# Optimization experiments

Measured on AMD Instinct MI355X. Metric: run time of the kernel, lower is better.

The kernel has to match this reference:

```python
import jax, jax.numpy as jnp
import numpy as np

N_NODES = 50000
N_EDGES = 800000
NODE_IN = 16
NODE_OUT = 3
H = 128
N_LAYERS = 3


def setup_inputs() -> dict:
    key = jax.random.key(0)
    ks = jax.random.split(key, 16)
    s = 0.05
    inp = {
        "x": jax.random.normal(ks[0], (N_NODES, NODE_IN), dtype=jnp.float32),
        "edge_index": jax.random.randint(ks[1], (2, N_EDGES), 0, N_NODES, dtype=jnp.int64),
        # encoder / decoder
        "enc_w": jax.random.normal(ks[2], (NODE_IN, H), dtype=jnp.float32) * s,
        "enc_b": jnp.zeros((H,), dtype=jnp.float32),
        "dec_w": jax.random.normal(ks[3], (H, NODE_OUT), dtype=jnp.float32) * s,
        "dec_b": jnp.zeros((NODE_OUT,), dtype=jnp.float32),
        # 3 processor layers, edge MLP: Linear(2H,H) -> ReLU -> Linear(H,H)
        "edge_w1": jax.random.normal(ks[4], (N_LAYERS, 2 * H, H), dtype=jnp.float32) * s,
        "edge_b1": jnp.zeros((N_LAYERS, H), dtype=jnp.float32),
        "edge_w2": jax.random.normal(ks[5], (N_LAYERS, H, H), dtype=jnp.float32) * s,
        "edge_b2": jnp.zeros((N_LAYERS, H), dtype=jnp.float32),
        # node MLP: Linear(2H,H) -> ReLU -> Linear(H,H)
        "node_w1": jax.random.normal(ks[6], (N_LAYERS, 2 * H, H), dtype=jnp.float32) * s,
        "node_b1": jnp.zeros((N_LAYERS, H), dtype=jnp.float32),
        "node_w2": jax.random.normal(ks[7], (N_LAYERS, H, H), dtype=jnp.float32) * s,
        "node_b2": jnp.zeros((N_LAYERS, H), dtype=jnp.float32),
    }
    return inp


def reference(x, edge_index, enc_w, enc_b, dec_w, dec_b,
              edge_w1, edge_b1, edge_w2, edge_b2,
              node_w1, node_b1, node_w2, node_b2):
    row = edge_index[0]  # source nodes
    col = edge_index[1]  # destination nodes
    h = x @ enc_w + enc_b  # [N, H]
    for l in range(N_LAYERS):
        # EdgeModel: cat(src, dest) -> MLP
        e_in = jnp.concatenate([h[row], h[col]], axis=1)  # [E, 2H]
        e = jnp.maximum(e_in @ edge_w1[l] + edge_b1[l], 0.0) @ edge_w2[l] + edge_b2[l]  # [E, H]
        # NodeModel: scatter_add messages by col, cat with x -> MLP
        agg = jax.ops.segment_sum(e, col, num_segments=h.shape[0])  # [N, H]
        n_in = jnp.concatenate([h, agg], axis=1)  # [N, 2H]
        h_upd = jnp.maximum(n_in @ node_w1[l] + node_b1[l], 0.0) @ node_w2[l] + node_b2[l]
        h = h + h_upd  # residual
    return h @ dec_w + dec_b  # [N, NODE_OUT]
```

## Files before the change

### kernel.cpp

```cpp
#include <hip/hip_runtime.h>
#include <hip/hip_bf16.h>
#include <stdint.h>

#define N_NODES 50000
#define N_EDGES 800000
#define HID 128
#define NODE_IN 16
#define NODE_OUT 3
#define NODE_TILES 782
#define SCAN_BLOCKS 196
#define EDGE_BLOCKS 3125
#define MFOLD_BLOCKS 192
#define DG 32
#define DBLOCKS 1563

typedef __attribute__((ext_vector_type(8))) short short8;
typedef __attribute__((ext_vector_type(4))) float f32x4;
typedef __attribute__((ext_vector_type(4))) unsigned int u32x4;

__device__ __forceinline__ unsigned short f2bf(float f) {
    union { float f; unsigned int u; } v; v.f = f;
    unsigned int u = v.u;
    u += 0x7fff + ((u >> 16) & 1);
    return (unsigned short)(u >> 16);
}
__device__ __forceinline__ float bf2f(unsigned short s) {
    union { unsigned int u; float f; } v; v.u = ((unsigned int)s) << 16;
    return v.f;
}
__device__ __forceinline__ float bfu_lo(unsigned int u) {
    union { unsigned int u; float f; } v; v.u = u << 16; return v.f;
}
__device__ __forceinline__ float bfu_hi(unsigned int u) {
    union { unsigned int u; float f; } v; v.u = u & 0xffff0000u; return v.f;
}
__device__ __forceinline__ unsigned int cvt_pk_bf16(float lo, float hi) {
    unsigned int r;
    asm("v_cvt_pk_bf16_f32 %0, %1, %2" : "=v"(r) : "v"(lo), "v"(hi));
    return r;
}

__global__ __launch_bounds__(256) void k1_hist_mfold(
    const int* __restrict__ colp, int* __restrict__ cnt, int* __restrict__ rank,
    const float* __restrict__ edge_w2, const float* __restrict__ node_w1,
    const float* __restrict__ edge_b2,
    float* __restrict__ Mtmp, float* __restrict__ Vtmp) {
    int b = blockIdx.x, t = threadIdx.x;
    if (b < EDGE_BLOCKS) {
        int e = b * 256 + t;
        rank[e] = atomicAdd(&cnt[colp[e]], 1);
    } else {
        int d = (b - EDGE_BLOCKS) * 256 + t;
        int L = d / 16384, rem = d & 16383;
        int k = rem >> 7, n = rem & 127;
        const float* w2  = edge_w2 + (size_t)L * 16384;
        const float* w1b = node_w1 + (size_t)L * 32768 + 16384;
        float acc = 0.f;
        #pragma unroll 4
        for (int j = 0; j < 128; j++) acc += w2[k * 128 + j] * w1b[j * 128 + n];
        Mtmp[d] = acc;
        if (k == 0) {
            const float* b2 = edge_b2 + (size_t)L * 128;
            float vv = 0.f;
            #pragma unroll 4
            for (int j = 0; j < 128; j++) vv += b2[j] * w1b[j * 128 + n];
            Vtmp[L * 128 + n] = vv;
        }
    }
}

__global__ __launch_bounds__(256) void k2a_scan1_swizzle(
    const int* __restrict__ cnt, int* __restrict__ ex, int* __restrict__ bsums,
    const float* __restrict__ edge_w1, const float* __restrict__ node_w1,
    const float* __restrict__ node_w2, const float* __restrict__ Mtmp,
    unsigned short* __restrict__ swz) {
    __shared__ int s[256];
    int b = blockIdx.x, t = threadIdx.x;
    if (b < SCAN_BLOCKS) {
        int i = b * 256 + t;
        int v = (i < N_NODES) ? cnt[i] : 0;
        s[t] = v;
        __syncthreads();
        for (int off = 1; off < 256; off <<= 1) {
            int u = (t >= off) ? s[t - off] : 0;
            __syncthreads();
            s[t] += u;
            __syncthreads();
        }
        if (i < N_NODES) ex[i] = s[t] - v;
        if (t == 255) bsums[b] = s[255];
    } else {
        for (int d = (b - SCAN_BLOCKS) * 256 + t; d < 3 * 98304;
             d += (gridDim.x - SCAN_BLOCKS) * 256) {
            int L = d / 98304;
            int rem = d - L * 98304;
            unsigned short* base = swz + L * 98304;
            if (rem < 32768) {
                const float* w1 = edge_w1 + (size_t)L * 32768;
                int j = rem & 7, ll = (rem >> 3) & 63, tt = rem >> 9;
                int nt = tt & 15, kt = tt >> 4;
                int k = kt * 32 + ((ll >> 4) << 3) + j;
                int cc = nt * 16 + (ll & 15);
                float v = (cc < 128) ? w1[k * 128 + cc] : w1[(128 + k) * 128 + (cc - 128)];
                base[rem] = f2bf(v);
            } else if (rem < 49152) {
            } else if (rem < 81920) {
                int d2 = rem - 49152;
                int j = d2 & 7, ll = (d2 >> 3) & 63, tt = d2 >> 9;
                int nt = tt & 7, kt = tt >> 3;
                int k = kt * 32 + ((ll >> 4) << 3) + j, n = (nt << 4) + (ll & 15);
                float v = (k < 128) ? node_w1[(size_t)L * 32768 + k * 128 + n]
                                    : Mtmp[(size_t)L * 16384 + (k - 128) * 128 + n];
                base[rem] = f2bf(v);
            } else {
                int d2 = rem - 81920;
                const float* src = node_w2 + (size_t)L * 16384;
                int j = d2 & 7, ll = (d2 >> 3) & 63, tt = d2 >> 9;
                int nt = tt & 7, kt = tt >> 3;
                int k = kt * 32 + ((ll >> 4) << 3) + j, n = (nt << 4) + (ll & 15);
                base[rem] = f2bf(src[k * 128 + n]);
            }
        }
    }
}

__global__ __launch_bounds__(256) void k3a_scatter(
    const int* __restrict__ rowp, const int* __restrict__ colp,
    const int* __restrict__ ex, const int* __restrict__ bsums,
    const int* __restrict__ rank, int* __restrict__ rsrt,
    int* __restrict__ ex2) {
    __shared__ int sc[256];
    __shared__ int ls[SCAN_BLOCKS];
    int t = threadIdx.x;
    int v = (t < SCAN_BLOCKS) ? bsums[t] : 0;
    sc[t] = v;
    __syncthreads();
    for (int off = 1; off < 256; off <<= 1) {
        int u = (t >= off) ? sc[t - off] : 0;
        __syncthreads();
        sc[t] += u;
        __syncthreads();
    }
    if (t < SCAN_BLOCKS) ls[t] = sc[t] - v;
    __syncthreads();

    int b = blockIdx.x;
    if (b < SCAN_BLOCKS) {
        int i = b * 256 + t;
        if (i < N_NODES) ex2[i] = ex[i] + ls[b];
    }

    int e = b * 256 + t;
    if (e >= N_EDGES) return;
    int c = colp[e];
    int pos = ex[c] + ls[c >> 8] + rank[e];
    rsrt[pos] = rowp[e];
}

__global__ __launch_bounds__(256, 4) void k3b_encoder_sd(
    const float* __restrict__ x, const float* __restrict__ enc_w, const float* __restrict__ enc_b,
    const unsigned short* __restrict__ w1c, const float* __restrict__ eb1,
    unsigned short* __restrict__ h,
    unsigned short* __restrict__ S, unsigned short* __restrict__ D)
{
    __shared__ float wts[NODE_IN * HID];
    __shared__ float bts[HID];
    __shared__ float xs[64][NODE_IN];
    __shared__ unsigned short hs[64][136];
    int t = threadIdx.x, wave = t >> 6, l = t & 63, q = l >> 4, l16 = l & 15;
    int n0 = blockIdx.x * 64;
    int nt0s = wave * 4;

    for (int i = t; i < NODE_IN * HID; i += 256) wts[i] = enc_w[i];
    if (t < HID) bts[t] = enc_b[t];
    for (int i = t; i < 64 * NODE_IN; i += 256) {
        int nl = i >> 4, ii = i & 15;
        int n = n0 + nl;
        xs[nl][ii] = (n < N_NODES) ? x[n * NODE_IN + ii] : 0.f;
    }
    short8 wr[4][4];
    #pragma unroll
    for (int kt = 0; kt < 4; kt++)
        #pragma unroll
        for (int i = 0; i < 4; i++)
            wr[kt][i] = *(const short8*)(w1c + ((kt * 16 + nt0s + i) * 64 + l) * 8);
    __syncthreads();

    for (int o = t; o < 64 * HID; o += 256) {
        int nl = o >> 7, cc = o & 127;
        float acc = bts[cc];
        #pragma unroll
        for (int i = 0; i < NODE_IN; i++) acc += xs[nl][i] * wts[i * HID + cc];
        unsigned short hb = f2bf(acc);
        hs[nl][cc] = hb;
        int n = n0 + nl;
        if (n < N_NODES) h[n * HID + cc] = hb;
    }
    __syncthreads();

    f32x4 acc[4][4];
    #pragma unroll
    for (int g = 0; g < 4; g++)
        #pragma unroll
        for (int i = 0; i < 4; i++) acc[g][i] = (f32x4){0.f, 0.f, 0.f, 0.f};
    #pragma unroll
    for (int kt = 0; kt < 4; kt++) {
        #pragma unroll
        for (int g = 0; g < 4; g++) {
            short8 a = *(const short8*)&hs[g * 16 + l16][kt * 32 + q * 8];
            #pragma unroll
            for (int i = 0; i < 4; i++)
                acc[g][i] = __builtin_amdgcn_mfma_f32_16x16x32_bf16(a, wr[kt][i], acc[g][i], 0, 0, 0);
        }
    }
    #pragma unroll
    for (int i = 0; i < 4; i++) {
        int cc = (nt0s + i) * 16 + l16;
        float badd = 0.f;
        if (cc >= 128) badd = eb1[cc - 128];
        #pragma unroll
        for (int g = 0; g < 4; g++)
            #pragma unroll
            for (int r = 0; r < 4; r++) {
                int n = n0 + g * 16 + q * 4 + r;
                if (n < N_NODES) {
                    unsigned short v = f2bf(acc[g][i][r] + badd);
                    if (cc < 128) S[n * HID + cc] = v;
                    else          D[n * HID + (cc - 128)] = v;
                }
            }
    }
}

__global__ __launch_bounds__(256, 8) void edge_kernel(
    const unsigned short* __restrict__ S, const unsigned short* __restrict__ D,
    const int* __restrict__ rsrt, const int* __restrict__ ex2,
    float* __restrict__ aggH)
{
    int t = threadIdx.x;
    int g16 = t >> 4, ch = t & 15;

    const int q = DBLOCKS / 8, r = DBLOCKS % 8;
    int xcd = blockIdx.x & 7, slot = blockIdx.x >> 3;
    int cntx = q + (xcd < r);
    if (slot >= cntx) return;
    int myb = xcd * q + (xcd < r ? xcd : r) + slot;

    int dbase = myb * DG + g16 * 2;

    #pragma unroll
    for (int di = 0; di < 2; di++) {
        int d = dbase + di;
        if (d >= N_NODES) break;
        int e0 = ex2[d];
        int e1 = (d + 1 < N_NODES) ? ex2[d + 1] : N_EDGES;

        short8 dv = *(const short8*)(D + (size_t)d * HID + ch * 8);
        float dr[8];
        #pragma unroll
        for (int p = 0; p < 4; p++) {
            unsigned int ud = ((const unsigned int*)&dv)[p];
            dr[2 * p]     = bfu_lo(ud);
            dr[2 * p + 1] = bfu_hi(ud);
        }

        float a[8];
        #pragma unroll
        for (int j = 0; j < 8; j++) a[j] = 0.f;

        int e = e0;
        short8 sv_n = (short8){0,0,0,0,0,0,0,0};
        if (e < e1) {
            int rn = rsrt[e];
            sv_n = *(const short8*)(S + (size_t)rn * HID + ch * 8);
        }
        while (e < e1) {
            short8 sv = sv_n;
            int en = e + 1;
            if (en < e1) {
                int rn = rsrt[en];
                sv_n = *(const short8*)(S + (size_t)rn * HID + ch * 8);
            }
            #pragma unroll
            for (int p = 0; p < 4; p++) {
                unsigned int us = ((const unsigned int*)&sv)[p];
                float v0 = bfu_lo(us) + dr[2 * p];
                float v1 = bfu_hi(us) + dr[2 * p + 1];
                v0 = v0 > 0.f ? v0 : 0.f;
                v1 = v1 > 0.f ? v1 : 0.f;
                a[2 * p]     += v0;
                a[2 * p + 1] += v1;
            }
            e = en;
        }

        f32x4* dst = (f32x4*)(aggH + (size_t)d * HID + ch * 8);
        dst[0] = (f32x4){a[0], a[1], a[2], a[3]};
        dst[1] = (f32x4){a[4], a[5], a[6], a[7]};
    }
}

template<int LAST>
__global__ __launch_bounds__(256, 4) void node_kernel(
    unsigned short* __restrict__ h, float* __restrict__ aggH, const int* __restrict__ cnt,
    const unsigned short* __restrict__ w1m_s, const float* __restrict__ b1,
    const float* __restrict__ vfold,
    const unsigned short* __restrict__ w2s, const float* __restrict__ b2,
    const unsigned short* __restrict__ w1c_next, const float* __restrict__ eb1n,
    unsigned short* __restrict__ S, unsigned short* __restrict__ D,
    const float* __restrict__ dec_w, const float* __restrict__ dec_b, float* __restrict__ out)
{
    __shared__ unsigned short in_h[64][136];
    __shared__ unsigned short in_a[64][136];
    __shared__ int cnt_s[64];
    __shared__ float dw[HID * NODE_OUT];
    __shared__ float db[NODE_OUT];
    int t = threadIdx.x, wave = t >> 6, l = t & 63, q = l >> 4, l16 = l & 15;
    int nt0 = wave * 2, nt0s = wave * 4;
    int n0 = blockIdx.x * 64;

    if (LAST) {
        for (int i = t; i < HID * NODE_OUT; i += 256) dw[i] = dec_w[i];
        if (t < NODE_OUT) db[t] = dec_b[t];
    }

    #pragma unroll
    for (int it = 0; it < 8; it++) {
        int g = it * 256 + t;
        int nl = g >> 5, sub = g & 31, half = sub >> 4, li = sub & 15;
        int n = n0 + nl;
        short8 v = (short8){0, 0, 0, 0, 0, 0, 0, 0};
        if (n < N_NODES) {
            if (half == 0) {
                v = *(const short8*)(h + n * HID + li * 8);
            } else {
                const float* ap = aggH + n * HID + li * 8;
                f32x4 a0 = *(const f32x4*)ap, a1 = *(const f32x4*)(ap + 4);
                unsigned int* vp = (unsigned int*)&v;
                vp[0] = cvt_pk_bf16(a0[0], a0[1]);
                vp[1] = cvt_pk_bf16(a0[2], a0[3]);
                vp[2] = cvt_pk_bf16(a1[0], a1[1]);
                vp[3] = cvt_pk_bf16(a1[2], a1[3]);
            }
        }
        if (half == 0) *(short8*)&in_h[nl][li * 8] = v;
        else           *(short8*)&in_a[nl][li * 8] = v;
    }
    if (t < 64) cnt_s[t] = (n0 + t < N_NODES) ? cnt[n0 + t] : 0;
    __syncthreads();

    float b1r0 = b1[nt0 * 16 + l16], b1r1 = b1[(nt0 + 1) * 16 + l16];
    float vr0 = vfold[nt0 * 16 + l16], vr1 = vfold[(nt0 + 1) * 16 + l16];
    float b2r0 = b2[nt0 * 16 + l16], b2r1 = b2[(nt0 + 1) * 16 + l16];

    f32x4 acc[4][2];
    #pragma unroll
    for (int g = 0; g < 4; g++)
        #pragma unroll
        for (int j = 0; j < 2; j++) acc[g][j] = (f32x4){0.f, 0.f, 0.f, 0.f};
    #pragma unroll
    for (int kt = 0; kt < 8; kt++) {
        short8 b0 = *(const short8*)(w1m_s + ((kt * 8 + nt0)     * 64 + l) * 8);
        short8 b1v = *(const short8*)(w1m_s + ((kt * 8 + nt0 + 1) * 64 + l) * 8);
        #pragma unroll
        for (int g = 0; g < 4; g++) {
            short8 a = (kt < 4) ? *(const short8*)&in_h[g * 16 + l16][kt * 32 + q * 8]
                                : *(const short8*)&in_a[g * 16 + l16][(kt - 4) * 32 + q * 8];
            acc[g][0] = __builtin_amdgcn_mfma_f32_16x16x32_bf16(a, b0, acc[g][0], 0, 0, 0);
            acc[g][1] = __builtin_amdgcn_mfma_f32_16x16x32_bf16(a, b1v, acc[g][1], 0, 0, 0);
        }
    }
    __syncthreads();

    #pragma unroll
    for (int j = 0; j < 2; j++) {
        float bv = j ? b1r1 : b1r0;
        float vv = j ? vr1 : vr0;
        #pragma unroll
        for (int g = 0; g < 4; g++)
            #pragma unroll
            for (int r = 0; r < 4; r++) {
                int m2 = g * 16 + q * 4 + r;
                float v = acc[g][j][r] + bv + (float)cnt_s[m2] * vv;
                v = v > 0.f ? v : 0.f;
                in_a[m2][(nt0 + j) * 16 + l16] = f2bf(v);
            }
    }
    __syncthreads();

    f32x4 acc2[4][2];
    #pragma unroll
    for (int g = 0; g < 4; g++)
        #pragma unroll
        for (int j = 0; j < 2; j++) acc2[g][j] = (f32x4){0.f, 0.f, 0.f, 0.f};
    #pragma unroll
    for (int kt = 0; kt < 4; kt++) {
        short8 b0 = *(const short8*)(w2s + ((kt * 8 + nt0)     * 64 + l) * 8);
        short8 b1v = *(const short8*)(w2s + ((kt * 8 + nt0 + 1) * 64 + l) * 8);
        #pragma unroll
        for (int g = 0; g < 4; g++) {
            short8 a = *(const short8*)&in_a[g * 16 + l16][kt * 32 + q * 8];
            acc2[g][0] = __builtin_amdgcn_mfma_f32_16x16x32_bf16(a, b0, acc2[g][0], 0, 0, 0);
            acc2[g][1] = __builtin_amdgcn_mfma_f32_16x16x32_bf16(a, b1v, acc2[g][1], 0, 0, 0);
        }
    }
    #pragma unroll
    for (int j = 0; j < 2; j++) {
        float bv = j ? b2r1 : b2r0;
        #pragma unroll
        for (int g = 0; g < 4; g++)
            #pragma unroll
            for (int r = 0; r < 4; r++) {
                float v = acc2[g][j][r] + bv;
                int m2 = g * 16 + q * 4 + r;
                int n = n0 + m2;
                if (n < N_NODES) {
                    int c = (nt0 + j) * 16 + l16;
                    unsigned short nh = f2bf(bf2f(in_h[m2][c]) + v);
                    if (!LAST) h[n * HID + c] = nh;
                    in_h[m2][c] = nh;
                }
            }
    }
    __syncthreads();

    if (!LAST) {
        #pragma unroll
        for (int p = 0; p < 2; p++) {
            short8 wr[4][2];
            #pragma unroll
            for (int kt = 0; kt < 4; kt++) {
                wr[kt][0] = *(const short8*)(w1c_next + ((kt * 16 + nt0s + p * 2)     * 64 + l) * 8);
                wr[kt][1] = *(const short8*)(w1c_next + ((kt * 16 + nt0s + p * 2 + 1) * 64 + l) * 8);
            }
            f32x4 accs[4][2];
            #pragma unroll
            for (int g = 0; g < 4; g++)
                #pragma unroll
                for (int i = 0; i < 2; i++) accs[g][i] = (f32x4){0.f, 0.f, 0.f, 0.f};
            #pragma unroll
            for (int kt = 0; kt < 4; kt++) {
                #pragma unroll
                for (int g = 0; g < 4; g++) {
                    short8 a = *(const short8*)&in_h[g * 16 + l16][kt * 32 + q * 8];
                    accs[g][0] = __builtin_amdgcn_mfma_f32_16x16x32_bf16(a, wr[kt][0], accs[g][0], 0, 0, 0);
                    accs[g][1] = __builtin_amdgcn_mfma_f32_16x16x32_bf16(a, wr[kt][1], accs[g][1], 0, 0, 0);
                }
            }
            #pragma unroll
            for (int i = 0; i < 2; i++) {
                int c = (nt0s + p * 2 + i) * 16 + l16;
                float badd = 0.f;
                if (c >= 128) badd = eb1n[c - 128];
                #pragma unroll
                for (int g = 0; g < 4; g++)
                    #pragma unroll
                    for (int r = 0; r < 4; r++) {
                        int n = n0 + g * 16 + q * 4 + r;
                        if (n < N_NODES) {
                            unsigned short v = f2bf(accs[g][i][r] + badd);
                            if (c < 128) S[n * HID + c] = v;
                            else         D[n * HID + (c - 128)] = v;
                        }
                    }
            }
        }
    } else {
        if (t < 64 * NODE_OUT) {
            int nl = t / 3, o = t - 3 * nl;
            int n = n0 + nl;
            if (n < N_NODES) {
                float a = db[o];
                #pragma unroll 4
                for (int k = 0; k < HID; k++) a += bf2f(in_h[nl][k]) * dw[k * 3 + o];
                out[n * 3 + o] = a;
            }
        }
    }
}

extern "C" void kernel_launch(void* const* d_in, const int* in_sizes, int n_in,
                              void* d_out, int out_size, void* d_ws, size_t ws_size,
                              hipStream_t stream) {
    const float* x       = (const float*)d_in[0];
    const int*   ei      = (const int*)d_in[1];
    const float* enc_w   = (const float*)d_in[2];
    const float* enc_b   = (const float*)d_in[3];
    const float* dec_w   = (const float*)d_in[4];
    const float* dec_b   = (const float*)d_in[5];
    const float* edge_w1 = (const float*)d_in[6];
    const float* edge_b1 = (const float*)d_in[7];
    const float* edge_w2 = (const float*)d_in[8];
    const float* edge_b2 = (const float*)d_in[9];
    const float* node_w1 = (const float*)d_in[10];
    const float* node_b1 = (const float*)d_in[11];
    const float* node_w2 = (const float*)d_in[12];
    const float* node_b2 = (const float*)d_in[13];

    char* ws = (char*)d_ws;
    unsigned short* h    = (unsigned short*)ws;
    float*          aggH = (float*)(ws + 12800000);
    unsigned short* swz  = (unsigned short*)(ws + 38400000);
    int* cnt             = (int*)(ws + 38989824);
    int* ex              = (int*)(ws + 39189824);
    int* bsums           = (int*)(ws + 39389824);
    int* rsrt            = (int*)(ws + 39390848);
    unsigned short* Sbuf = (unsigned short*)(ws + 45790848);
    unsigned short* Dbuf = (unsigned short*)(ws + 58590848);
    float* Mtmp          = (float*)(ws + 71390848);
    float* Vtmp          = (float*)(ws + 71587456);
    int* ex2             = (int*)(ws + 71588992);
    int* rank            = (int*)(ws + 58590848);

    const int* rowp = ei;
    const int* colp = ei + N_EDGES;

    hipMemsetAsync(cnt, 0, (size_t)N_NODES * 4, stream);

    k1_hist_mfold<<<EDGE_BLOCKS + MFOLD_BLOCKS, 256, 0, stream>>>(
        colp, cnt, rank, edge_w2, node_w1, edge_b2, Mtmp, Vtmp);
    k2a_scan1_swizzle<<<SCAN_BLOCKS + 288, 256, 0, stream>>>(cnt, ex, bsums, edge_w1,
                                                             node_w1, node_w2, Mtmp, swz);
    k3a_scatter<<<3125, 256, 0, stream>>>(rowp, colp, ex, bsums, rank, rsrt, ex2);
    k3b_encoder_sd<<<NODE_TILES, 256, 0, stream>>>(x, enc_w, enc_b, swz ,
                                                   edge_b1 , h,
                                                   Sbuf, Dbuf);

    for (int L = 0; L < 3; L++) {
        unsigned short* base = swz + (size_t)L * 98304;
        unsigned short* next = swz + (size_t)(L + 1) * 98304;
        edge_kernel<<<1568, 256, 0, stream>>>(Sbuf, Dbuf, rsrt, ex2, aggH);
        if (L < 2) {
            node_kernel<0><<<NODE_TILES, 256, 0, stream>>>(
                h, aggH, cnt,
                base + 49152, node_b1 + (size_t)L * HID, Vtmp + (size_t)L * HID,
                base + 81920, node_b2 + (size_t)L * HID,
                next, edge_b1 + (size_t)(L + 1) * HID, Sbuf, Dbuf, dec_w, dec_b, (float*)d_out);
        } else {
            node_kernel<1><<<NODE_TILES, 256, 0, stream>>>(
                h, aggH, cnt,
                base + 49152, node_b1 + (size_t)L * HID, Vtmp + (size_t)L * HID,
                base + 81920, node_b2 + (size_t)L * HID,
                base , edge_b1 , Sbuf, Dbuf, dec_w, dec_b, (float*)d_out);
        }
    }
}
```

Before: 385.2 us.

## Fuse encoder into histogram kernel, merge scatter with S/D projection, retune edge gather

Moves the encoder linear layer into the first histogram/weight-fold launch and merges the CSR scatter with the S/D projection MFMA kernel, removing one launch and letting independent block types run concurrently. The edge aggregation kernel now assigns one destination node per 16-lane group instead of two, doubling the block count. It also replaces the single-edge prefetch with a two-edge-deep software pipeline. The rank buffer moves to its own workspace region so it no longer aliases Dbuf, which is now written in the same launch that reads rank. The cost is that the encoder output h must round-trip through global memory before the S/D projection reads it back.

```diff
diff --git a/kernel.cpp b/kernel.cpp
--- a/kernel.cpp
+++ b/kernel.cpp
@@ -11,8 +11,8 @@
 #define SCAN_BLOCKS 196
 #define EDGE_BLOCKS 3125
 #define MFOLD_BLOCKS 192
-#define DG 32
-#define DBLOCKS 1563
+#define DGB 16
+#define EDBLOCKS 3125
 
 typedef __attribute__((ext_vector_type(8))) short short8;
 typedef __attribute__((ext_vector_type(4))) float f32x4;
@@ -40,16 +40,21 @@
     return r;
 }
 
-__global__ __launch_bounds__(256) void k1_hist_mfold(
+__global__ __launch_bounds__(256) void k1_fused(
     const int* __restrict__ colp, int* __restrict__ cnt, int* __restrict__ rank,
     const float* __restrict__ edge_w2, const float* __restrict__ node_w1,
     const float* __restrict__ edge_b2,
-    float* __restrict__ Mtmp, float* __restrict__ Vtmp) {
+    float* __restrict__ Mtmp, float* __restrict__ Vtmp,
+    const float* __restrict__ x, const float* __restrict__ enc_w,
+    const float* __restrict__ enc_b, unsigned short* __restrict__ h) {
+    __shared__ float wts[NODE_IN * HID];
+    __shared__ float bts[HID];
+    __shared__ float xs[64][NODE_IN];
     int b = blockIdx.x, t = threadIdx.x;
     if (b < EDGE_BLOCKS) {
         int e = b * 256 + t;
         rank[e] = atomicAdd(&cnt[colp[e]], 1);
-    } else {
+    } else if (b < EDGE_BLOCKS + MFOLD_BLOCKS) {
         int d = (b - EDGE_BLOCKS) * 256 + t;
         int L = d / 16384, rem = d & 16383;
         int k = rem >> 7, n = rem & 127;
@@ -65,6 +70,25 @@
             #pragma unroll 4
             for (int j = 0; j < 128; j++) vv += b2[j] * w1b[j * 128 + n];
             Vtmp[L * 128 + n] = vv;
+        }
+    } else {
+        int b2 = b - EDGE_BLOCKS - MFOLD_BLOCKS;
+        int n0 = b2 * 64;
+        for (int i = t; i < NODE_IN * HID; i += 256) wts[i] = enc_w[i];
+        if (t < HID) bts[t] = enc_b[t];
+        for (int i = t; i < 64 * NODE_IN; i += 256) {
+            int nl = i >> 4, ii = i & 15;
+            int n = n0 + nl;
+            xs[nl][ii] = (n < N_NODES) ? x[n * NODE_IN + ii] : 0.f;
+        }
+        __syncthreads();
+        for (int o = t; o < 64 * HID; o += 256) {
+            int nl = o >> 7, cc = o & 127;
+            float acc = bts[cc];
+            #pragma unroll
+            for (int i = 0; i < NODE_IN; i++) acc += xs[nl][i] * wts[i * HID + cc];
+            int n = n0 + nl;
+            if (n < N_NODES) h[n * HID + cc] = f2bf(acc);
         }
     }
 }
@@ -124,111 +148,90 @@
     }
 }
 
-__global__ __launch_bounds__(256) void k3a_scatter(
+__global__ __launch_bounds__(256) void k3_scatter_sd(
     const int* __restrict__ rowp, const int* __restrict__ colp,
     const int* __restrict__ ex, const int* __restrict__ bsums,
-    const int* __restrict__ rank, int* __restrict__ rsrt,
-    int* __restrict__ ex2) {
+    const int* __restrict__ rank, int* __restrict__ rsrt, int* __restrict__ ex2,
+    const unsigned short* __restrict__ h, const unsigned short* __restrict__ w1c,
+    const float* __restrict__ eb1,
+    unsigned short* __restrict__ S, unsigned short* __restrict__ D) {
     __shared__ int sc[256];
     __shared__ int ls[SCAN_BLOCKS];
-    int t = threadIdx.x;
-    int v = (t < SCAN_BLOCKS) ? bsums[t] : 0;
-    sc[t] = v;
-    __syncthreads();
-    for (int off = 1; off < 256; off <<= 1) {
-        int u = (t >= off) ? sc[t - off] : 0;
+    __shared__ unsigned short hs[64][136];
+    int b = blockIdx.x, t = threadIdx.x;
+    if (b < EDGE_BLOCKS) {
+        int v = (t < SCAN_BLOCKS) ? bsums[t] : 0;
+        sc[t] = v;
         __syncthreads();
-        sc[t] += u;
+        for (int off = 1; off < 256; off <<= 1) {
+            int u = (t >= off) ? sc[t - off] : 0;
+            __syncthreads();
+            sc[t] += u;
+            __syncthreads();
+        }
+        if (t < SCAN_BLOCKS) ls[t] = sc[t] - v;
         __syncthreads();
-    }
-    if (t < SCAN_BLOCKS) ls[t] = sc[t] - v;
-    __syncthreads();
-
-    int b = blockIdx.x;
-    if (b < SCAN_BLOCKS) {
-        int i = b * 256 + t;
-        if (i < N_NODES) ex2[i] = ex[i] + ls[b];
-    }
-
-    int e = b * 256 + t;
-    if (e >= N_EDGES) return;
-    int c = colp[e];
-    int pos = ex[c] + ls[c >> 8] + rank[e];
-    rsrt[pos] = rowp[e];
-}
-
-__global__ __launch_bounds__(256, 4) void k3b_encoder_sd(
-    const float* __restrict__ x, const float* __restrict__ enc_w, const float* __restrict__ enc_b,
-    const unsigned short* __restrict__ w1c, const float* __restrict__ eb1,
-    unsigned short* __restrict__ h,
-    unsigned short* __restrict__ S, unsigned short* __restrict__ D)
-{
-    __shared__ float wts[NODE_IN * HID];
-    __shared__ float bts[HID];
-    __shared__ float xs[64][NODE_IN];
-    __shared__ unsigned short hs[64][136];
-    int t = threadIdx.x, wave = t >> 6, l = t & 63, q = l >> 4, l16 = l & 15;
-    int n0 = blockIdx.x * 64;
-    int nt0s = wave * 4;
-
-    for (int i = t; i < NODE_IN * HID; i += 256) wts[i] = enc_w[i];
-    if (t < HID) bts[t] = enc_b[t];
-    for (int i = t; i < 64 * NODE_IN; i += 256) {
-        int nl = i >> 4, ii = i & 15;
-        int n = n0 + nl;
-        xs[nl][ii] = (n < N_NODES) ? x[n * NODE_IN + ii] : 0.f;
-    }
-    short8 wr[4][4];
-    #pragma unroll
-    for (int kt = 0; kt < 4; kt++)
-        #pragma unroll
-        for (int i = 0; i < 4; i++)
-            wr[kt][i] = *(const short8*)(w1c + ((kt * 16 + nt0s + i) * 64 + l) * 8);
-    __syncthreads();
-
-    for (int o = t; o < 64 * HID; o += 256) {
-        int nl = o >> 7, cc = o & 127;
-        float acc = bts[cc];
-        #pragma unroll
-        for (int i = 0; i < NODE_IN; i++) acc += xs[nl][i] * wts[i * HID + cc];
-        unsigned short hb = f2bf(acc);
-        hs[nl][cc] = hb;
-        int n = n0 + nl;
-        if (n < N_NODES) h[n * HID + cc] = hb;
-    }
-    __syncthreads();
-
-    f32x4 acc[4][4];
-    #pragma unroll
-    for (int g = 0; g < 4; g++)
-        #pragma unroll
-        for (int i = 0; i < 4; i++) acc[g][i] = (f32x4){0.f, 0.f, 0.f, 0.f};
-    #pragma unroll
-    for (int kt = 0; kt < 4; kt++) {
-        #pragma unroll
-        for (int g = 0; g < 4; g++) {
-            short8 a = *(const short8*)&hs[g * 16 + l16][kt * 32 + q * 8];
+
+        if (b < SCAN_BLOCKS) {
+            int i = b * 256 + t;
+            if (i < N_NODES) ex2[i] = ex[i] + ls[b];
+        }
+        int e = b * 256 + t;
+        int c = colp[e];
+        int pos = ex[c] + ls[c >> 8] + rank[e];
+        rsrt[pos] = rowp[e];
+    } else {
+        int b2 = b - EDGE_BLOCKS;
+        int wave = t >> 6, l = t & 63, q = l >> 4, l16 = l & 15;
+        int nt0s = wave * 4;
+        int n0 = b2 * 64;
+        for (int i = t; i < 64 * 16; i += 256) {
+            int nl = i >> 4, li = i & 15;
+            int n = n0 + nl;
+            short8 v = (short8){0, 0, 0, 0, 0, 0, 0, 0};
+            if (n < N_NODES) v = *(const short8*)(h + (size_t)n * HID + li * 8);
+            *(short8*)&hs[nl][li * 8] = v;
+        }
+        short8 wr[4][4];
+        #pragma unroll
+        for (int kt = 0; kt < 4; kt++)
             #pragma unroll
             for (int i = 0; i < 4; i++)
-                acc[g][i] = __builtin_amdgcn_mfma_f32_16x16x32_bf16(a, wr[kt][i], acc[g][i], 0, 0, 0);
-        }
-    }
-    #pragma unroll
-    for (int i = 0; i < 4; i++) {
-        int cc = (nt0s + i) * 16 + l16;
-        float badd = 0.f;
-        if (cc >= 128) badd = eb1[cc - 128];
+                wr[kt][i] = *(const short8*)(w1c + ((kt * 16 + nt0s + i) * 64 + l) * 8);
+        __syncthreads();
+
+        f32x4 acc[4][4];
         #pragma unroll
         for (int g = 0; g < 4; g++)
             #pragma unroll
-            for (int r = 0; r < 4; r++) {
-                int n = n0 + g * 16 + q * 4 + r;
-                if (n < N_NODES) {
-                    unsigned short v = f2bf(acc[g][i][r] + badd);
-                    if (cc < 128) S[n * HID + cc] = v;
-                    else          D[n * HID + (cc - 128)] = v;
+            for (int i = 0; i < 4; i++) acc[g][i] = (f32x4){0.f, 0.f, 0.f, 0.f};
+        #pragma unroll
+        for (int kt = 0; kt < 4; kt++) {
+            #pragma unroll
+            for (int g = 0; g < 4; g++) {
+                short8 a = *(const short8*)&hs[g * 16 + l16][kt * 32 + q * 8];
+                #pragma unroll
+                for (int i = 0; i < 4; i++)
+                    acc[g][i] = __builtin_amdgcn_mfma_f32_16x16x32_bf16(a, wr[kt][i], acc[g][i], 0, 0, 0);
+            }
+        }
+        #pragma unroll
+        for (int i = 0; i < 4; i++) {
+            int cc = (nt0s + i) * 16 + l16;
+            float badd = 0.f;
+            if (cc >= 128) badd = eb1[cc - 128];
+            #pragma unroll
+            for (int g = 0; g < 4; g++)
+                #pragma unroll
+                for (int r = 0; r < 4; r++) {
+                    int n = n0 + g * 16 + q * 4 + r;
+                    if (n < N_NODES) {
+                        unsigned short v = f2bf(acc[g][i][r] + badd);
+                        if (cc < 128) S[n * HID + cc] = v;
+                        else          D[n * HID + (cc - 128)] = v;
+                    }
                 }
-            }
+        }
     }
 }
 
@@ -240,64 +243,65 @@
     int t = threadIdx.x;
     int g16 = t >> 4, ch = t & 15;
 
-    const int q = DBLOCKS / 8, r = DBLOCKS % 8;
+    const int q = EDBLOCKS / 8, r = EDBLOCKS % 8;
     int xcd = blockIdx.x & 7, slot = blockIdx.x >> 3;
     int cntx = q + (xcd < r);
     if (slot >= cntx) return;
     int myb = xcd * q + (xcd < r ? xcd : r) + slot;
 
-    int dbase = myb * DG + g16 * 2;
-
-    #pragma unroll
-    for (int di = 0; di < 2; di++) {
-        int d = dbase + di;
-        if (d >= N_NODES) break;
-        int e0 = ex2[d];
-        int e1 = (d + 1 < N_NODES) ? ex2[d + 1] : N_EDGES;
-
-        short8 dv = *(const short8*)(D + (size_t)d * HID + ch * 8);
-        float dr[8];
+    int d = myb * DGB + g16;
+    int e0 = ex2[d];
+    int e1 = (d < N_NODES - 1) ? ex2[d + 1] : N_EDGES;
+
+    short8 dv = *(const short8*)(D + (size_t)d * HID + ch * 8);
+    float dr[8];
+    #pragma unroll
+    for (int p = 0; p < 4; p++) {
+        unsigned int ud = ((const unsigned int*)&dv)[p];
+        dr[2 * p]     = bfu_lo(ud);
+        dr[2 * p + 1] = bfu_hi(ud);
+    }
+
+    float a[8];
+    #pragma unroll
+    for (int j = 0; j < 8; j++) a[j] = 0.f;
+
+    auto ldS = [&](int e) -> short8 {
+        int rn = rsrt[e];
+        return *(const short8*)(S + (size_t)rn * HID + ch * 8);
+    };
+    auto accum = [&](const short8& sv) {
         #pragma unroll
         for (int p = 0; p < 4; p++) {
-            unsigned int ud = ((const unsigned int*)&dv)[p];
-            dr[2 * p]     = bfu_lo(ud);
-            dr[2 * p + 1] = bfu_hi(ud);
-        }
-
-        float a[8];
-        #pragma unroll
-        for (int j = 0; j < 8; j++) a[j] = 0.f;
-
-        int e = e0;
-        short8 sv_n = (short8){0,0,0,0,0,0,0,0};
-        if (e < e1) {
-            int rn = rsrt[e];
-            sv_n = *(const short8*)(S + (size_t)rn * HID + ch * 8);
-        }
-        while (e < e1) {
-            short8 sv = sv_n;
-            int en = e + 1;
-            if (en < e1) {
-                int rn = rsrt[en];
-                sv_n = *(const short8*)(S + (size_t)rn * HID + ch * 8);
-            }
-            #pragma unroll
-            for (int p = 0; p < 4; p++) {
-                unsigned int us = ((const unsigned int*)&sv)[p];
-                float v0 = bfu_lo(us) + dr[2 * p];
-                float v1 = bfu_hi(us) + dr[2 * p + 1];
-                v0 = v0 > 0.f ? v0 : 0.f;
-                v1 = v1 > 0.f ? v1 : 0.f;
-                a[2 * p]     += v0;
-                a[2 * p + 1] += v1;
-            }
-            e = en;
-        }
-
-        f32x4* dst = (f32x4*)(aggH + (size_t)d * HID + ch * 8);
-        dst[0] = (f32x4){a[0], a[1], a[2], a[3]};
-        dst[1] = (f32x4){a[4], a[5], a[6], a[7]};
-    }
+            unsigned int us = ((const unsigned int*)&sv)[p];
+            float v0 = bfu_lo(us) + dr[2 * p];
+            float v1 = bfu_hi(us) + dr[2 * p + 1];
+            v0 = v0 > 0.f ? v0 : 0.f;
+            v1 = v1 > 0.f ? v1 : 0.f;
+            a[2 * p]     += v0;
+            a[2 * p + 1] += v1;
+        }
+    };
+
+    int e = e0;
+    short8 s0 = (short8){0, 0, 0, 0, 0, 0, 0, 0};
+    short8 s1 = s0;
+    if (e < e1)     s0 = ldS(e);
+    if (e + 1 < e1) s1 = ldS(e + 1);
+    for (; e + 2 < e1; e += 2) {
+        short8 n0v = ldS(e + 2);
+        short8 n1v = (e + 3 < e1) ? ldS(e + 3) : (short8){0, 0, 0, 0, 0, 0, 0, 0};
+        accum(s0);
+        accum(s1);
+        s0 = n0v;
+        s1 = n1v;
+    }
+    if (e < e1)     accum(s0);
+    if (e + 1 < e1) accum(s1);
+
+    f32x4* dst = (f32x4*)(aggH + (size_t)d * HID + ch * 8);
+    dst[0] = (f32x4){a[0], a[1], a[2], a[3]};
+    dst[1] = (f32x4){a[4], a[5], a[6], a[7]};
 }
 
 template<int LAST>
@@ -510,26 +514,26 @@
     float* Mtmp          = (float*)(ws + 71390848);
     float* Vtmp          = (float*)(ws + 71587456);
     int* ex2             = (int*)(ws + 71588992);
-    int* rank            = (int*)(ws + 58590848);
+    int* rank            = (int*)(ws + 72000000);
 
     const int* rowp = ei;
     const int* colp = ei + N_EDGES;
 
     hipMemsetAsync(cnt, 0, (size_t)N_NODES * 4, stream);
 
-    k1_hist_mfold<<<EDGE_BLOCKS + MFOLD_BLOCKS, 256, 0, stream>>>(
-        colp, cnt, rank, edge_w2, node_w1, edge_b2, Mtmp, Vtmp);
+    k1_fused<<<EDGE_BLOCKS + MFOLD_BLOCKS + NODE_TILES, 256, 0, stream>>>(
+        colp, cnt, rank, edge_w2, node_w1, edge_b2, Mtmp, Vtmp,
+        x, enc_w, enc_b, h);
     k2a_scan1_swizzle<<<SCAN_BLOCKS + 288, 256, 0, stream>>>(cnt, ex, bsums, edge_w1,
                                                              node_w1, node_w2, Mtmp, swz);
-    k3a_scatter<<<3125, 256, 0, stream>>>(rowp, colp, ex, bsums, rank, rsrt, ex2);
-    k3b_encoder_sd<<<NODE_TILES, 256, 0, stream>>>(x, enc_w, enc_b, swz ,
-                                                   edge_b1 , h,
-                                                   Sbuf, Dbuf);
+    k3_scatter_sd<<<EDGE_BLOCKS + NODE_TILES, 256, 0, stream>>>(
+        rowp, colp, ex, bsums, rank, rsrt, ex2,
+        h, swz , edge_b1 , Sbuf, Dbuf);
 
     for (int L = 0; L < 3; L++) {
         unsigned short* base = swz + (size_t)L * 98304;
         unsigned short* next = swz + (size_t)(L + 1) * 98304;
-        edge_kernel<<<1568, 256, 0, stream>>>(Sbuf, Dbuf, rsrt, ex2, aggH);
+        edge_kernel<<<3128, 256, 0, stream>>>(Sbuf, Dbuf, rsrt, ex2, aggH);
         if (L < 2) {
             node_kernel<0><<<NODE_TILES, 256, 0, stream>>>(
                 h, aggH, cnt,
```

After: 364.9 us. 5.3% less time.
